# Performance work log

Hardware: AMD Instinct MI355X
Metric: run time of the kernel (lower is better)

Reference implementation:

```python
import jax, jax.numpy as jnp
import numpy as np

N = 100000
E = 1600000
IN_F, HID, OUT_F = 256, 128, 64


def setup_inputs() -> dict:
    key = jax.random.key(0)
    k_x, k_e, k_w1, k_w2, k_b1, k_b2 = jax.random.split(key, 6)
    x = jax.random.normal(k_x, (N, IN_F), dtype=jnp.float32)
    edge_index = jax.random.randint(k_e, (2, E), 0, N, dtype=jnp.int32)
    # GCNConv params: lin has no bias in PyG; separate additive bias per layer.
    W1 = jax.random.normal(k_w1, (IN_F, HID), dtype=jnp.float32) / np.sqrt(IN_F)
    b1 = jax.random.normal(k_b1, (HID,), dtype=jnp.float32) * 0.01
    W2 = jax.random.normal(k_w2, (HID, OUT_F), dtype=jnp.float32) / np.sqrt(HID)
    b2 = jax.random.normal(k_b2, (OUT_F,), dtype=jnp.float32) * 0.01
    return {"x": x, "edge_index": edge_index, "W1": W1, "b1": b1, "W2": W2, "b2": b2}


def _gcn_norm(edge_index, num_nodes):
    # add self loops (improved=False -> weight 1.0), symmetric normalization
    loop = jnp.arange(num_nodes, dtype=edge_index.dtype)
    src = jnp.concatenate([edge_index[0], loop])
    dst = jnp.concatenate([edge_index[1], loop])
    w = jnp.ones(src.shape[0], dtype=jnp.float32)
    deg = jax.ops.segment_sum(w, dst, num_segments=num_nodes)
    dinv = jnp.where(deg > 0, jax.lax.rsqrt(deg), 0.0)
    norm = dinv[src] * w * dinv[dst]
    return src, dst, norm


def _gcn_layer(h, W, b, src, dst, norm, num_nodes):
    h = h @ W                               # [N, out]
    msg = h[src] * norm[:, None]            # [E+N, out] gather + scale
    out = jax.ops.segment_sum(msg, dst, num_segments=num_nodes)  # scatter-add
    return out + b


def reference(x, edge_index, W1, b1, W2, b2):
    # dropout is identity in eval mode
    src, dst, norm = _gcn_norm(edge_index, N)
    h = _gcn_layer(x, W1, b1, src, dst, norm, N)
    h = jax.nn.relu(h)
    out = _gcn_layer(h, W2, b2, src, dst, norm, N)
    return out
```

## Files before the change

### kernel.cpp

```cpp
#include <hip/hip_runtime.h>
#include <hip/hip_bf16.h>

#define N_NODES 100000
#define N_EDGES 1600000
#define IN_FEAT 256
#define HID_F   128
#define OUT_FT  64

#define NBUK   256
#define NPB    391
#define BUKCAP 8192
#define EPB    4096
#define G_BIN  ((N_EDGES + EPB - 1) / EPB)
#define G_GEMM ((N_NODES + 127) / 128)
#define G_CAST ((IN_FEAT * HID_F + HID_F * OUT_FT + 255) / 256)

typedef unsigned short u16;
typedef __attribute__((ext_vector_type(8))) unsigned short u16x8;
typedef __attribute__((ext_vector_type(8))) short short8;
typedef __attribute__((ext_vector_type(4))) float f32x4;

static __device__ inline u16 f2bf(float f) {
    __hip_bfloat16 h = __float2bfloat16(f);
    return *reinterpret_cast<u16*>(&h);
}
static __device__ inline float bf2f(u16 u) {
    union { unsigned u; float f; } c;
    c.u = ((unsigned)u) << 16;
    return c.f;
}


__global__ __launch_bounds__(256) void k_bin(const int* __restrict__ srcA,
                                             const int* __restrict__ dstA,
                                             int* __restrict__ gcur, int2* __restrict__ pairs,
                                             const float* __restrict__ W1,
                                             const float* __restrict__ W2,
                                             u16* __restrict__ W1t, u16* __restrict__ W2t) {
    if (blockIdx.x >= G_BIN) {
        int idx = (blockIdx.x - G_BIN) * 256 + threadIdx.x;
        if (idx < IN_FEAT * HID_F) {
            int k = idx / HID_F, n = idx % HID_F;
            W1t[n * IN_FEAT + k] = f2bf(W1[idx]);
        } else {
            int e2 = idx - IN_FEAT * HID_F;
            if (e2 < HID_F * OUT_FT) {
                int k = e2 / OUT_FT, n = e2 % OUT_FT;
                W2t[n * HID_F + k] = f2bf(W2[e2]);
            }
        }
        return;
    }
    __shared__ int lh[NBUK];
    int t = threadIdx.x;
    int e0 = blockIdx.x * EPB;
    if (t < NBUK) lh[t] = 0;
    __syncthreads();
#pragma unroll
    for (int i = 0; i < EPB / 256; i++) {
        int e = e0 + i * 256 + t;
        if (e < N_EDGES) atomicAdd(&lh[dstA[e] / NPB], 1);
    }
    __syncthreads();
    if (t < NBUK) {
        int c = lh[t];
        lh[t] = atomicAdd(&gcur[t], c);
    }
    __syncthreads();
#pragma unroll
    for (int i = 0; i < EPB / 256; i++) {
        int e = e0 + i * 256 + t;
        if (e < N_EDGES) {
            int d = dstA[e];
            int b = d / NPB;
            int p = atomicAdd(&lh[b], 1);
            if (p < BUKCAP) pairs[(size_t)b * BUKCAP + p] = make_int2(srcA[e], d);
        }
    }
}


__global__ __launch_bounds__(256) void k_bukscan(const int* __restrict__ gcur,
                                                 int* __restrict__ bbase) {
    __shared__ int sm[256];
    int t = threadIdx.x;
    int v = gcur[t];
    sm[t] = v;
    __syncthreads();
    for (int o = 1; o < 256; o <<= 1) {
        int u = (t >= o) ? sm[t - o] : 0;
        __syncthreads();
        sm[t] += u;
        __syncthreads();
    }
    bbase[t] = sm[t] - v;
    if (t == NBUK - 1) bbase[NBUK] = sm[t];
}


__global__ __launch_bounds__(256) void k_fillB(const int2* __restrict__ pairs,
                                               const int* __restrict__ gcnt,
                                               const int* __restrict__ bbase,
                                               int* __restrict__ offsets,
                                               float* __restrict__ dinv,
                                               int* __restrict__ csr) {
    __shared__ int hist[NPB];
    __shared__ int sm[256];
    int b = blockIdx.x, t = threadIdx.x;
    int nbase = b * NPB;
    int nn = min(NPB, N_NODES - nbase);
    int cnt = gcnt[b];
    int ebase = bbase[b];
    const int2* pb = pairs + (size_t)b * BUKCAP;

    for (int i = t; i < NPB; i += 256) hist[i] = 0;
    __syncthreads();
    for (int i = t; i < cnt; i += 256) atomicAdd(&hist[pb[i].y - nbase], 1);
    __syncthreads();

    int base2 = t * 2;
    int c0 = (base2 < NPB) ? hist[base2] : 0;
    int c1 = (base2 + 1 < NPB) ? hist[base2 + 1] : 0;
    int s = c0 + c1;
    sm[t] = s;
    __syncthreads();
    for (int o = 1; o < 256; o <<= 1) {
        int u = (t >= o) ? sm[t - o] : 0;
        __syncthreads();
        sm[t] += u;
        __syncthreads();
    }
    int run = ebase + sm[t] - s;
    __syncthreads();
    int cc[2] = {c0, c1};
#pragma unroll
    for (int q = 0; q < 2; q++) {
        int n = base2 + q;
        if (n < nn) {
            int g = nbase + n;
            offsets[g] = run;
            dinv[g] = rsqrtf((float)(cc[q] + 1));
            hist[n] = run;
            run += cc[q];
        }
    }
    __syncthreads();
    for (int i = t; i < cnt; i += 256) {
        int2 e = pb[i];
        int p = atomicAdd(&hist[e.y - nbase], 1);
        csr[p] = e.x;
    }
    if (b == NBUK - 1 && t == 0) offsets[N_NODES] = N_EDGES;
}


__global__ __launch_bounds__(256) void k_gemm1(const float* __restrict__ A,
                                               const u16* __restrict__ Bt,
                                               const float* __restrict__ dinv,
                                               u16* __restrict__ C) {
    __shared__ u16 As[128][40];
    __shared__ u16 Bs[128][40];
    int tid = threadIdx.x;
    int wv = tid >> 6, lane = tid & 63;
    int m16 = lane & 15, quad = lane >> 4;
    int row0 = blockIdx.x * 128;
    int r = tid >> 1, h = tid & 1;
    int grow_s = row0 + r;
    bool rok = grow_s < N_NODES;

    f32x4 acc[2][8];
#pragma unroll
    for (int i = 0; i < 2; i++)
#pragma unroll
        for (int j = 0; j < 8; j++) acc[i][j] = (f32x4)(0.f);

    for (int k0 = 0; k0 < IN_FEAT; k0 += 32) {
        f32x4 v0 = (f32x4)(0.f), v1 = v0, v2 = v0, v3 = v0;
        if (rok) {
            const f32x4* src = (const f32x4*)&A[(size_t)grow_s * IN_FEAT + k0 + h * 16];
            v0 = src[0]; v1 = src[1]; v2 = src[2]; v3 = src[3];
        }
        u16x8 p0, p1;
#pragma unroll
        for (int j = 0; j < 4; j++) {
            p0[j] = f2bf(v0[j]); p0[4 + j] = f2bf(v1[j]);
            p1[j] = f2bf(v2[j]); p1[4 + j] = f2bf(v3[j]);
        }
        *(u16x8*)&As[r][h * 16] = p0;
        *(u16x8*)&As[r][h * 16 + 8] = p1;
        const u16x8* bsrc = (const u16x8*)&Bt[(size_t)r * IN_FEAT + k0 + h * 16];
        *(u16x8*)&Bs[r][h * 16] = bsrc[0];
        *(u16x8*)&Bs[r][h * 16 + 8] = bsrc[1];
        __syncthreads();

        short8 af0 = *(const short8*)&As[32 * wv + m16][quad * 8];
        short8 af1 = *(const short8*)&As[32 * wv + 16 + m16][quad * 8];
#pragma unroll
        for (int ct = 0; ct < 8; ct++) {
            short8 bf = *(const short8*)&Bs[16 * ct + m16][quad * 8];
            acc[0][ct] = __builtin_amdgcn_mfma_f32_16x16x32_bf16(af0, bf, acc[0][ct], 0, 0, 0);
            acc[1][ct] = __builtin_amdgcn_mfma_f32_16x16x32_bf16(af1, bf, acc[1][ct], 0, 0, 0);
        }
        __syncthreads();
    }
#pragma unroll
    for (int rt = 0; rt < 2; rt++)
#pragma unroll
        for (int r4 = 0; r4 < 4; r4++) {
            int grow = row0 + 32 * wv + 16 * rt + quad * 4 + r4;
            if (grow < N_NODES) {
                float dv = dinv[grow];
#pragma unroll
                for (int ct = 0; ct < 8; ct++)
                    C[(size_t)grow * HID_F + 16 * ct + m16] = f2bf(acc[rt][ct][r4] * dv);
            }
        }
}


__global__ __launch_bounds__(256) void k_gemm2(const u16* __restrict__ A,
                                               const u16* __restrict__ Bt,
                                               const float* __restrict__ dinv,
                                               u16* __restrict__ C) {
    __shared__ u16 As[128][40];
    __shared__ u16 Bs[64][40];
    int tid = threadIdx.x;
    int wv = tid >> 6, lane = tid & 63;
    int m16 = lane & 15, quad = lane >> 4;
    int row0 = blockIdx.x * 128;
    int r = tid >> 1, h = tid & 1;
    int grow_s = row0 + r;
    bool rok = grow_s < N_NODES;
    int nb = tid >> 2, q = tid & 3;

    f32x4 acc[2][4];
#pragma unroll
    for (int i = 0; i < 2; i++)
#pragma unroll
        for (int j = 0; j < 4; j++) acc[i][j] = (f32x4)(0.f);

    for (int k0 = 0; k0 < HID_F; k0 += 32) {
        u16x8 a0 = (u16x8)(0), a1v = (u16x8)(0);
        if (rok) {
            const u16x8* src = (const u16x8*)&A[(size_t)grow_s * HID_F + k0 + h * 16];
            a0 = src[0]; a1v = src[1];
        }
        *(u16x8*)&As[r][h * 16] = a0;
        *(u16x8*)&As[r][h * 16 + 8] = a1v;
        *(u16x8*)&Bs[nb][q * 8] = *(const u16x8*)&Bt[(size_t)nb * HID_F + k0 + q * 8];
        __syncthreads();

        short8 af0 = *(const short8*)&As[32 * wv + m16][quad * 8];
        short8 af1 = *(const short8*)&As[32 * wv + 16 + m16][quad * 8];
#pragma unroll
        for (int ct = 0; ct < 4; ct++) {
            short8 bf = *(const short8*)&Bs[16 * ct + m16][quad * 8];
            acc[0][ct] = __builtin_amdgcn_mfma_f32_16x16x32_bf16(af0, bf, acc[0][ct], 0, 0, 0);
            acc[1][ct] = __builtin_amdgcn_mfma_f32_16x16x32_bf16(af1, bf, acc[1][ct], 0, 0, 0);
        }
        __syncthreads();
    }
#pragma unroll
    for (int rt = 0; rt < 2; rt++)
#pragma unroll
        for (int r4 = 0; r4 < 4; r4++) {
            int grow = row0 + 32 * wv + 16 * rt + quad * 4 + r4;
            if (grow < N_NODES) {
                float dv = dinv[grow];
#pragma unroll
                for (int ct = 0; ct < 4; ct++)
                    C[(size_t)grow * OUT_FT + 16 * ct + m16] = f2bf(acc[rt][ct][r4] * dv);
            }
        }
}


__global__ __launch_bounds__(256) void k_agg1(const u16* __restrict__ hs,
                                              const int* __restrict__ offsets,
                                              const int* __restrict__ csr,
                                              const float* __restrict__ dinv,
                                              const float* __restrict__ b,
                                              u16* __restrict__ out) {
    int wave = threadIdx.x >> 6;
    int lane = threadIdx.x & 63;
    int node = blockIdx.x * 4 + wave;
    if (node >= N_NODES) return;
    int g = lane >> 4;
    int fl = lane & 15;
    const int fo = fl * 8;
    int beg = offsets[node], end = offsets[node + 1];

    float acc[8];
#pragma unroll
    for (int i = 0; i < 8; i++) acc[i] = 0.f;

    int j = beg;
    for (; j + 8 <= end; j += 8) {
        int s0 = csr[j + g];
        int s1 = csr[j + 4 + g];
        u16x8 r0 = *(const u16x8*)&hs[(size_t)s0 * HID_F + fo];
        u16x8 r1 = *(const u16x8*)&hs[(size_t)s1 * HID_F + fo];
#pragma unroll
        for (int i = 0; i < 8; i++) acc[i] += bf2f(r0[i]) + bf2f(r1[i]);
    }
    for (; j < end; j += 4) {
        int idx = j + g;
        if (idx < end) {
            int s = csr[idx];
            u16x8 r0 = *(const u16x8*)&hs[(size_t)s * HID_F + fo];
#pragma unroll
            for (int i = 0; i < 8; i++) acc[i] += bf2f(r0[i]);
        }
    }
#pragma unroll
    for (int i = 0; i < 8; i++) {
        acc[i] += __shfl_xor(acc[i], 16, 64);
        acc[i] += __shfl_xor(acc[i], 32, 64);
    }
    u16x8 sr = *(const u16x8*)&hs[(size_t)node * HID_F + fo];
#pragma unroll
    for (int i = 0; i < 8; i++) acc[i] += bf2f(sr[i]);

    if (g == 0) {
        float dv = dinv[node];
        f32x4 b0 = *(const f32x4*)&b[fo];
        f32x4 b1 = *(const f32x4*)&b[fo + 4];
        u16x8 o;
#pragma unroll
        for (int i = 0; i < 4; i++) {
            o[i] = f2bf(fmaxf(dv * acc[i] + b0[i], 0.f));
            o[4 + i] = f2bf(fmaxf(dv * acc[4 + i] + b1[i], 0.f));
        }
        *(u16x8*)&out[(size_t)node * HID_F + fo] = o;
    }
}


__global__ __launch_bounds__(256) void k_agg2(const u16* __restrict__ hs,
                                              const int* __restrict__ offsets,
                                              const int* __restrict__ csr,
                                              const float* __restrict__ dinv,
                                              const float* __restrict__ b,
                                              float* __restrict__ out) {
    int wave = threadIdx.x >> 6;
    int lane = threadIdx.x & 63;
    int node = blockIdx.x * 4 + wave;
    if (node >= N_NODES) return;
    int g = lane >> 3;
    int fl = lane & 7;
    const int fo = fl * 8;
    int beg = offsets[node], end = offsets[node + 1];

    float acc[8];
#pragma unroll
    for (int i = 0; i < 8; i++) acc[i] = 0.f;

    int j = beg;
    for (; j + 16 <= end; j += 16) {
        int s0 = csr[j + g];
        int s1 = csr[j + 8 + g];
        u16x8 r0 = *(const u16x8*)&hs[(size_t)s0 * OUT_FT + fo];
        u16x8 r1 = *(const u16x8*)&hs[(size_t)s1 * OUT_FT + fo];
#pragma unroll
        for (int i = 0; i < 8; i++) acc[i] += bf2f(r0[i]) + bf2f(r1[i]);
    }
    for (; j < end; j += 8) {
        int idx = j + g;
        if (idx < end) {
            int s = csr[idx];
            u16x8 r0 = *(const u16x8*)&hs[(size_t)s * OUT_FT + fo];
#pragma unroll
            for (int i = 0; i < 8; i++) acc[i] += bf2f(r0[i]);
        }
    }
#pragma unroll
    for (int i = 0; i < 8; i++) {
        acc[i] += __shfl_xor(acc[i], 8, 64);
        acc[i] += __shfl_xor(acc[i], 16, 64);
        acc[i] += __shfl_xor(acc[i], 32, 64);
    }
    u16x8 sr = *(const u16x8*)&hs[(size_t)node * OUT_FT + fo];
#pragma unroll
    for (int i = 0; i < 8; i++) acc[i] += bf2f(sr[i]);

    if (g == 0) {
        float dv = dinv[node];
        f32x4 b0 = *(const f32x4*)&b[fo];
        f32x4 b1 = *(const f32x4*)&b[fo + 4];
        f32x4 o0, o1;
#pragma unroll
        for (int i = 0; i < 4; i++) {
            o0[i] = dv * acc[i] + b0[i];
            o1[i] = dv * acc[4 + i] + b1[i];
        }
        *(f32x4*)&out[(size_t)node * OUT_FT + fo] = o0;
        *(f32x4*)&out[(size_t)node * OUT_FT + fo + 4] = o1;
    }
}


extern "C" void kernel_launch(void* const* d_in, const int* in_sizes, int n_in,
                              void* d_out, int out_size, void* d_ws, size_t ws_size,
                              hipStream_t stream) {
    const float* x  = (const float*)d_in[0];
    const int*   ei = (const int*)d_in[1];
    const float* W1 = (const float*)d_in[2];
    const float* b1 = (const float*)d_in[3];
    const float* W2 = (const float*)d_in[4];
    const float* b2 = (const float*)d_in[5];
    float* out = (float*)d_out;

    char* ws = (char*)d_ws;
    int*   offsets = (int*)(ws + 0);
    float* dinv    = (float*)(ws + 400512);
    int*   csr     = (int*)(ws + 800512);
    u16*   W1t     = (u16*)(ws + 7200512);
    u16*   W2t     = (u16*)(ws + 7266048);
    int*   gcur    = (int*)(ws + 7282432);
    int*   bbase   = (int*)(ws + 7283456);
    u16*   hs1     = (u16*)(ws + 7284608);
    u16*   a1      = (u16*)(ws + 32884608);
    int2*  pairs   = (int2*)(ws + 32884608);
    u16*   hs2     = hs1;

    const int* srcA = ei;
    const int* dstA = ei + N_EDGES;

    hipMemsetAsync(gcur, 0, NBUK * sizeof(int), stream);

    k_bin<<<G_BIN + G_CAST, 256, 0, stream>>>(srcA, dstA, gcur, pairs, W1, W2, W1t, W2t);
    k_bukscan<<<1, 256, 0, stream>>>(gcur, bbase);
    k_fillB<<<NBUK, 256, 0, stream>>>(pairs, gcur, bbase, offsets, dinv, csr);

    k_gemm1<<<G_GEMM, 256, 0, stream>>>(x, W1t, dinv, hs1);
    k_agg1<<<(N_NODES + 3) / 4, 256, 0, stream>>>(hs1, offsets, csr, dinv, b1, a1);
    k_gemm2<<<G_GEMM, 256, 0, stream>>>(a1, W2t, dinv, hs2);
    k_agg2<<<(N_NODES + 3) / 4, 256, 0, stream>>>(hs2, offsets, csr, dinv, b2, out);
}
```

Measured before the change: 356.4 us.

## Fuse bucket scan into fillB and process two nodes per wave in aggregation

Removes the single-block bucket scan kernel by having every fillB block redundantly scan the 256 bucket counts in shared memory. The aggregation kernels now map two nodes per wave (half-wave each), using two accumulator sets and four gathers per iteration with a shallower shuffle reduction. The intent is to cut launch overhead and cross-lane reduction cost, and to raise memory-level parallelism. In exchange, per-node lane parallelism is halved, so high-degree nodes may take longer.

```diff
diff --git a/kernel.cpp b/kernel.cpp
--- a/kernel.cpp
+++ b/kernel.cpp
@@ -14,6 +14,7 @@
 #define G_BIN  ((N_EDGES + EPB - 1) / EPB)
 #define G_GEMM ((N_NODES + 127) / 128)
 #define G_CAST ((IN_FEAT * HID_F + HID_F * OUT_FT + 255) / 256)
+#define G_AGG  ((N_NODES + 7) / 8)
 
 typedef unsigned short u16;
 typedef __attribute__((ext_vector_type(8))) unsigned short u16x8;
@@ -80,37 +81,31 @@
 }
 
 
-__global__ __launch_bounds__(256) void k_bukscan(const int* __restrict__ gcur,
-                                                 int* __restrict__ bbase) {
-    __shared__ int sm[256];
-    int t = threadIdx.x;
-    int v = gcur[t];
-    sm[t] = v;
-    __syncthreads();
-    for (int o = 1; o < 256; o <<= 1) {
-        int u = (t >= o) ? sm[t - o] : 0;
-        __syncthreads();
-        sm[t] += u;
-        __syncthreads();
-    }
-    bbase[t] = sm[t] - v;
-    if (t == NBUK - 1) bbase[NBUK] = sm[t];
-}
-
-
 __global__ __launch_bounds__(256) void k_fillB(const int2* __restrict__ pairs,
                                                const int* __restrict__ gcnt,
-                                               const int* __restrict__ bbase,
                                                int* __restrict__ offsets,
                                                float* __restrict__ dinv,
                                                int* __restrict__ csr) {
     __shared__ int hist[NPB];
     __shared__ int sm[256];
+    __shared__ int s_ebase;
     int b = blockIdx.x, t = threadIdx.x;
     int nbase = b * NPB;
     int nn = min(NPB, N_NODES - nbase);
+
+    int gv = gcnt[t];
+    sm[t] = gv;
+    __syncthreads();
+    for (int o = 1; o < 256; o <<= 1) {
+        int u = (t >= o) ? sm[t - o] : 0;
+        __syncthreads();
+        sm[t] += u;
+        __syncthreads();
+    }
+    if (t == b) s_ebase = sm[t] - gv;
+    __syncthreads();
+    int ebase = s_ebase;
     int cnt = gcnt[b];
-    int ebase = bbase[b];
     const int2* pb = pairs + (size_t)b * BUKCAP;
 
     for (int i = t; i < NPB; i += 256) hist[i] = 0;
@@ -122,6 +117,7 @@
     int c0 = (base2 < NPB) ? hist[base2] : 0;
     int c1 = (base2 + 1 < NPB) ? hist[base2 + 1] : 0;
     int s = c0 + c1;
+    __syncthreads();
     sm[t] = s;
     __syncthreads();
     for (int o = 1; o < 256; o <<= 1) {
@@ -283,53 +279,69 @@
                                               u16* __restrict__ out) {
     int wave = threadIdx.x >> 6;
     int lane = threadIdx.x & 63;
-    int node = blockIdx.x * 4 + wave;
+    int half = lane >> 5;
+    int node = blockIdx.x * 8 + wave * 2 + half;
     if (node >= N_NODES) return;
-    int g = lane >> 4;
-    int fl = lane & 15;
+    int gl = lane & 31;
+    int g = gl >> 4;
+    int fl = gl & 15;
     const int fo = fl * 8;
     int beg = offsets[node], end = offsets[node + 1];
 
-    float acc[8];
-#pragma unroll
-    for (int i = 0; i < 8; i++) acc[i] = 0.f;
+    float accA[8], accB[8];
+#pragma unroll
+    for (int i = 0; i < 8; i++) { accA[i] = 0.f; accB[i] = 0.f; }
 
     int j = beg;
     for (; j + 8 <= end; j += 8) {
         int s0 = csr[j + g];
-        int s1 = csr[j + 4 + g];
+        int s1 = csr[j + 2 + g];
+        int s2 = csr[j + 4 + g];
+        int s3 = csr[j + 6 + g];
         u16x8 r0 = *(const u16x8*)&hs[(size_t)s0 * HID_F + fo];
         u16x8 r1 = *(const u16x8*)&hs[(size_t)s1 * HID_F + fo];
-#pragma unroll
-        for (int i = 0; i < 8; i++) acc[i] += bf2f(r0[i]) + bf2f(r1[i]);
-    }
-    for (; j < end; j += 4) {
+        u16x8 r2 = *(const u16x8*)&hs[(size_t)s2 * HID_F + fo];
+        u16x8 r3 = *(const u16x8*)&hs[(size_t)s3 * HID_F + fo];
+#pragma unroll
+        for (int i = 0; i < 8; i++) {
+            accA[i] += bf2f(r0[i]) + bf2f(r1[i]);
+            accB[i] += bf2f(r2[i]) + bf2f(r3[i]);
+        }
+    }
+    if (j + 4 <= end) {
+        int s0 = csr[j + g];
+        int s1 = csr[j + 2 + g];
+        u16x8 r0 = *(const u16x8*)&hs[(size_t)s0 * HID_F + fo];
+        u16x8 r1 = *(const u16x8*)&hs[(size_t)s1 * HID_F + fo];
+#pragma unroll
+        for (int i = 0; i < 8; i++) accA[i] += bf2f(r0[i]) + bf2f(r1[i]);
+        j += 4;
+    }
+    for (; j < end; j += 2) {
         int idx = j + g;
         if (idx < end) {
             int s = csr[idx];
             u16x8 r0 = *(const u16x8*)&hs[(size_t)s * HID_F + fo];
 #pragma unroll
-            for (int i = 0; i < 8; i++) acc[i] += bf2f(r0[i]);
+            for (int i = 0; i < 8; i++) accB[i] += bf2f(r0[i]);
         }
     }
 #pragma unroll
     for (int i = 0; i < 8; i++) {
-        acc[i] += __shfl_xor(acc[i], 16, 64);
-        acc[i] += __shfl_xor(acc[i], 32, 64);
-    }
-    u16x8 sr = *(const u16x8*)&hs[(size_t)node * HID_F + fo];
-#pragma unroll
-    for (int i = 0; i < 8; i++) acc[i] += bf2f(sr[i]);
-
+        float v = accA[i] + accB[i];
+        v += __shfl_xor(v, 16, 64);
+        accA[i] = v;
+    }
     if (g == 0) {
+        u16x8 sr = *(const u16x8*)&hs[(size_t)node * HID_F + fo];
         float dv = dinv[node];
         f32x4 b0 = *(const f32x4*)&b[fo];
         f32x4 b1 = *(const f32x4*)&b[fo + 4];
         u16x8 o;
 #pragma unroll
         for (int i = 0; i < 4; i++) {
-            o[i] = f2bf(fmaxf(dv * acc[i] + b0[i], 0.f));
-            o[4 + i] = f2bf(fmaxf(dv * acc[4 + i] + b1[i], 0.f));
+            o[i]     = f2bf(fmaxf(dv * (accA[i]     + bf2f(sr[i]))     + b0[i], 0.f));
+            o[4 + i] = f2bf(fmaxf(dv * (accA[4 + i] + bf2f(sr[4 + i])) + b1[i], 0.f));
         }
         *(u16x8*)&out[(size_t)node * HID_F + fo] = o;
     }
@@ -344,54 +356,70 @@
                                               float* __restrict__ out) {
     int wave = threadIdx.x >> 6;
     int lane = threadIdx.x & 63;
-    int node = blockIdx.x * 4 + wave;
+    int half = lane >> 5;
+    int node = blockIdx.x * 8 + wave * 2 + half;
     if (node >= N_NODES) return;
-    int g = lane >> 3;
-    int fl = lane & 7;
+    int gl = lane & 31;
+    int g = gl >> 3;
+    int fl = gl & 7;
     const int fo = fl * 8;
     int beg = offsets[node], end = offsets[node + 1];
 
-    float acc[8];
-#pragma unroll
-    for (int i = 0; i < 8; i++) acc[i] = 0.f;
+    float accA[8], accB[8];
+#pragma unroll
+    for (int i = 0; i < 8; i++) { accA[i] = 0.f; accB[i] = 0.f; }
 
     int j = beg;
     for (; j + 16 <= end; j += 16) {
         int s0 = csr[j + g];
-        int s1 = csr[j + 8 + g];
+        int s1 = csr[j + 4 + g];
+        int s2 = csr[j + 8 + g];
+        int s3 = csr[j + 12 + g];
         u16x8 r0 = *(const u16x8*)&hs[(size_t)s0 * OUT_FT + fo];
         u16x8 r1 = *(const u16x8*)&hs[(size_t)s1 * OUT_FT + fo];
-#pragma unroll
-        for (int i = 0; i < 8; i++) acc[i] += bf2f(r0[i]) + bf2f(r1[i]);
-    }
-    for (; j < end; j += 8) {
+        u16x8 r2 = *(const u16x8*)&hs[(size_t)s2 * OUT_FT + fo];
+        u16x8 r3 = *(const u16x8*)&hs[(size_t)s3 * OUT_FT + fo];
+#pragma unroll
+        for (int i = 0; i < 8; i++) {
+            accA[i] += bf2f(r0[i]) + bf2f(r1[i]);
+            accB[i] += bf2f(r2[i]) + bf2f(r3[i]);
+        }
+    }
+    if (j + 8 <= end) {
+        int s0 = csr[j + g];
+        int s1 = csr[j + 4 + g];
+        u16x8 r0 = *(const u16x8*)&hs[(size_t)s0 * OUT_FT + fo];
+        u16x8 r1 = *(const u16x8*)&hs[(size_t)s1 * OUT_FT + fo];
+#pragma unroll
+        for (int i = 0; i < 8; i++) accA[i] += bf2f(r0[i]) + bf2f(r1[i]);
+        j += 8;
+    }
+    for (; j < end; j += 4) {
         int idx = j + g;
         if (idx < end) {
             int s = csr[idx];
             u16x8 r0 = *(const u16x8*)&hs[(size_t)s * OUT_FT + fo];
 #pragma unroll
-            for (int i = 0; i < 8; i++) acc[i] += bf2f(r0[i]);
+            for (int i = 0; i < 8; i++) accB[i] += bf2f(r0[i]);
         }
     }
 #pragma unroll
     for (int i = 0; i < 8; i++) {
-        acc[i] += __shfl_xor(acc[i], 8, 64);
-        acc[i] += __shfl_xor(acc[i], 16, 64);
-        acc[i] += __shfl_xor(acc[i], 32, 64);
-    }
-    u16x8 sr = *(const u16x8*)&hs[(size_t)node * OUT_FT + fo];
-#pragma unroll
-    for (int i = 0; i < 8; i++) acc[i] += bf2f(sr[i]);
-
+        float v = accA[i] + accB[i];
+        v += __shfl_xor(v, 8, 64);
+        v += __shfl_xor(v, 16, 64);
+        accA[i] = v;
+    }
     if (g == 0) {
+        u16x8 sr = *(const u16x8*)&hs[(size_t)node * OUT_FT + fo];
         float dv = dinv[node];
         f32x4 b0 = *(const f32x4*)&b[fo];
         f32x4 b1 = *(const f32x4*)&b[fo + 4];
         f32x4 o0, o1;
 #pragma unroll
         for (int i = 0; i < 4; i++) {
-            o0[i] = dv * acc[i] + b0[i];
-            o1[i] = dv * acc[4 + i] + b1[i];
+            o0[i] = dv * (accA[i]     + bf2f(sr[i]))     + b0[i];
+            o1[i] = dv * (accA[4 + i] + bf2f(sr[4 + i])) + b1[i];
         }
         *(f32x4*)&out[(size_t)node * OUT_FT + fo] = o0;
         *(f32x4*)&out[(size_t)node * OUT_FT + fo + 4] = o1;
@@ -417,7 +445,6 @@
     u16*   W1t     = (u16*)(ws + 7200512);
     u16*   W2t     = (u16*)(ws + 7266048);
     int*   gcur    = (int*)(ws + 7282432);
-    int*   bbase   = (int*)(ws + 7283456);
     u16*   hs1     = (u16*)(ws + 7284608);
     u16*   a1      = (u16*)(ws + 32884608);
     int2*  pairs   = (int2*)(ws + 32884608);
@@ -429,11 +456,10 @@
     hipMemsetAsync(gcur, 0, NBUK * sizeof(int), stream);
 
     k_bin<<<G_BIN + G_CAST, 256, 0, stream>>>(srcA, dstA, gcur, pairs, W1, W2, W1t, W2t);
-    k_bukscan<<<1, 256, 0, stream>>>(gcur, bbase);
-    k_fillB<<<NBUK, 256, 0, stream>>>(pairs, gcur, bbase, offsets, dinv, csr);
+    k_fillB<<<NBUK, 256, 0, stream>>>(pairs, gcur, offsets, dinv, csr);
 
     k_gemm1<<<G_GEMM, 256, 0, stream>>>(x, W1t, dinv, hs1);
-    k_agg1<<<(N_NODES + 3) / 4, 256, 0, stream>>>(hs1, offsets, csr, dinv, b1, a1);
+    k_agg1<<<G_AGG, 256, 0, stream>>>(hs1, offsets, csr, dinv, b1, a1);
     k_gemm2<<<G_GEMM, 256, 0, stream>>>(a1, W2t, dinv, hs2);
-    k_agg2<<<(N_NODES + 3) / 4, 256, 0, stream>>>(hs2, offsets, csr, dinv, b2, out);
-}
+    k_agg2<<<G_AGG, 256, 0, stream>>>(hs2, offsets, csr, dinv, b2, out);
+}
```

New measurement: 345.1 us. 1.03x faster.
